# Optimization experiments

Hardware: AMD Instinct MI355X
Metric: run time of the kernel (lower is better)

## Reference

```python
import jax, jax.numpy as jnp
import numpy as np

B, N, K, G = 8, 16384, 16, 4
D_OUT = 128
CQ = CV = 64            # cv must equal d_out//2 for the lpe reshape to work
CQG, CVG = CQ // G, CV // G
C_LPE = D_OUT // (2 * G)  # = CVG = 16
BN_EPS = 1e-5


def setup_inputs() -> dict:
    key = jax.random.key(0)
    ks = jax.random.split(key, 8)
    xyz = jax.random.normal(ks[0], (B, N, 3), dtype=jnp.float32)
    query = jax.random.normal(ks[1], (B, CQ, N), dtype=jnp.float32)
    value = jax.random.normal(ks[2], (B, CV, N, 1), dtype=jnp.float32)
    neigh_idx = jax.random.randint(ks[3], (B, N, K), 0, N, dtype=jnp.int64)
    idx_base = (jnp.arange(B, dtype=jnp.int64) * N).reshape(B, 1, 1)
    lpe_W = jax.random.normal(ks[4], (C_LPE, 10), dtype=jnp.float32) * 0.1
    lpe_b = jnp.zeros((C_LPE,), dtype=jnp.float32)
    bn_gamma = jnp.ones((C_LPE,), dtype=jnp.float32)
    bn_beta = jnp.zeros((C_LPE,), dtype=jnp.float32)
    bn_mean = jnp.zeros((C_LPE,), dtype=jnp.float32)
    bn_var = jnp.ones((C_LPE,), dtype=jnp.float32)
    return {"xyz": xyz, "query": query, "value": value,
            "neigh_idx": neigh_idx, "idx_base": idx_base,
            "lpe_W": lpe_W, "lpe_b": lpe_b, "bn_gamma": bn_gamma,
            "bn_beta": bn_beta, "bn_mean": bn_mean, "bn_var": bn_var}


def _gtl_forward(xyz, query, value, neigh_idx, idx_base,
                 lpe_W, lpe_b, bn_gamma, bn_beta, bn_mean, bn_var):
    b, n, _ = xyz.shape
    k = neigh_idx.shape[-1]
    lq = query.reshape(b, G, CQG, n)                       # [b,g,cqg,n]
    lv = value.reshape(b, G, CVG, n)                       # [b,g,cvg,n]
    xyz_g = jnp.broadcast_to(xyz[:, None].transpose(0, 1, 3, 2), (b, G, 3, n))
    # temp channels: key(cqg) | value(cvg) | xyz(3)
    temp = jnp.concatenate([lq, lv, xyz_g], axis=2)        # [b,g,c,n]
    c = temp.shape[2]
    # flat gather honoring idx_base (batch offsets into b*n)
    flat_idx = (neigh_idx + idx_base).reshape(-1)          # [b*n*k]
    pc_flat = temp.transpose(1, 0, 3, 2).reshape(G, b * n, c)
    feat = pc_flat[:, flat_idx, :].reshape(G, b, n, k, c)
    feat = feat.transpose(1, 0, 4, 2, 3)                   # [b,g,c,n,k]
    lk = feat[:, :, :CQG]                                  # [b,g,cqg,n,k]
    lv_n = feat[:, :, CQG:CQG + CVG]                       # [b,g,cvg,n,k]
    f_xyz = feat[:, :, -3:]                                # [b,g,3,n,k]
    # relative positional encoding -> [b,g,n,k,10]
    neighbor_xyz = f_xyz.transpose(0, 1, 3, 4, 2)          # [b,g,n,k,3]
    xyz_tile = jnp.broadcast_to(xyz[:, None, :, None, :], (b, G, n, k, 3))
    relative_xyz = xyz_tile - neighbor_xyz
    relative_dis = jnp.sqrt(jnp.sum(relative_xyz ** 2, axis=-1, keepdims=True))
    relf = jnp.concatenate([relative_dis, relative_xyz, xyz_tile, neighbor_xyz], axis=-1)
    # permute(0,4,2,1,3) then merge (g,k) -> conv input [b,10,n,g*k]
    relf = relf.transpose(0, 4, 2, 1, 3).reshape(b, 10, n, G * k)
    y = jnp.einsum('oc,bcnm->bonm', lpe_W, relf) + lpe_b[None, :, None, None]
    inv_std = bn_gamma / jnp.sqrt(bn_var + BN_EPS)
    y = (y - bn_mean[None, :, None, None]) * inv_std[None, :, None, None] \
        + bn_beta[None, :, None, None]
    y = jax.nn.relu(y)
    f_enc = y.reshape(b, C_LPE, n, G, k).transpose(0, 3, 1, 2, 4)  # [b,g,cvg,n,k]
    # elementwise attention over neighbors
    la = jax.nn.softmax(jnp.sum(lq[..., None] * lk, axis=2), axis=-1)  # [b,g,n,k]
    lv_cat = jnp.concatenate([lv_n, f_enc], axis=2)        # [b,g,2*cvg,n,k]
    out = jnp.sum(la[:, :, None] * lv_cat, axis=-1).reshape(b, -1, n, 1)
    # attention centrality: scatter-add over neighbor indices
    idx_flat = jnp.broadcast_to(neigh_idx[:, None], (b, G, n, k)).reshape(b, G, n * k)
    att_flat = la.reshape(b, G, n * k)
    centrality = jnp.zeros((b, G, n), dtype=la.dtype).at[
        jnp.arange(b)[:, None, None], jnp.arange(G)[None, :, None], idx_flat
    ].add(att_flat)
    return out, f_enc, centrality


def reference(xyz, query, value, neigh_idx, idx_base,
              lpe_W, lpe_b, bn_gamma, bn_beta, bn_mean, bn_var):
    return _gtl_forward(xyz, query, value, neigh_idx, idx_base,
                        lpe_W, lpe_b, bn_gamma, bn_beta, bn_mean, bn_var)
```

## Files before the change

### kernel.cpp

```cpp
#include <hip/hip_runtime.h>

#define B_    8
#define N_    16384
#define K_    16
#define G_    4
#define CQ_   64
#define CV_   64
#define CQG_  16
#define CVG_  16
#define CLPE_ 16
#define NT_   (B_*G_*N_)

typedef float f4v __attribute__((ext_vector_type(4)));

static __device__ __forceinline__ void nt_store4(float* p, float a, float b,
                                                 float c, float d) {
    f4v v = {a, b, c, d};
    __builtin_nontemporal_store(v, (f4v*)p);
}
static __device__ __forceinline__ void nt_store1(float* p, float a) {
    __builtin_nontemporal_store(a, p);
}

__global__ __launch_bounds__(256) void gtl_prep(
    const float* __restrict__ query,
    const float* __restrict__ value,
    const float* __restrict__ xyz,
    float4* __restrict__ qT4,
    float4* __restrict__ vT4,
    float4* __restrict__ xyz4,
    float*  __restrict__ cent)
{
    __shared__ float sq[CQG_][68];
    __shared__ float sv[CVG_][68];

    const int t    = threadIdx.x;
    const int bg   = blockIdx.x >> 8;
    const int tile = blockIdx.x & 255;
    const int n0   = tile << 6;
    const int g    = bg & (G_ - 1);
    const int b    = bg >> 2;

    const int row = t >> 6;
    const int col = t & 63;

    const float* qb = query + (size_t)b*CQ_*N_ + (size_t)g*CQG_*N_ + n0;
    const float* vb = value + (size_t)b*CV_*N_ + (size_t)g*CVG_*N_ + n0;

    #pragma unroll
    for (int cc = 0; cc < 4; ++cc) {
        const int c = (cc << 2) + row;
        sq[c][col] = qb[(size_t)c*N_ + col];
        sv[c][col] = vb[(size_t)c*N_ + col];
    }

    if (t < 64) {
        cent[(size_t)bg*N_ + n0 + t] = 0.f;
        if (g == 0) {
            const size_t pp = (size_t)b*N_ + n0 + t;
            xyz4[pp] = make_float4(xyz[pp*3+0], xyz[pp*3+1], xyz[pp*3+2], 0.f);
        }
    }

    __syncthreads();

    const int p    = t >> 2;
    const int quad = t & 3;
    const int cb   = quad << 2;
    const float4 oq = make_float4(sq[cb+0][p], sq[cb+1][p], sq[cb+2][p], sq[cb+3][p]);
    const float4 ov = make_float4(sv[cb+0][p], sv[cb+1][p], sv[cb+2][p], sv[cb+3][p]);
    const size_t o = ((size_t)bg*N_ + n0 + p)*4 + quad;
    qT4[o] = oq;
    vT4[o] = ov;
}

__global__ __launch_bounds__(256) void gtl_main(
    const float*  __restrict__ qT,
    const float*  __restrict__ vT,
    const float4* __restrict__ xyz4,
    const int*    __restrict__ nidx,
    const float*  __restrict__ lpeW,
    const float*  __restrict__ lpeB,
    const float*  __restrict__ bnG,
    const float*  __restrict__ bnB,
    const float*  __restrict__ bnM,
    const float*  __restrict__ bnV,
    float* __restrict__ out,
    float* __restrict__ fenc,
    float* __restrict__ cent)
{
    __shared__ float4 sA[CLPE_];
    __shared__ float4 sB[CLPE_];

    const int t = threadIdx.x;
    if (t < CLPE_) {
        const float scale = bnG[t] * rsqrtf(bnV[t] + 1e-5f);
        const float shift = (lpeB[t] - bnM[t]) * scale + bnB[t];
        const float w0 = lpeW[t*10+0];
        const float w1 = lpeW[t*10+1], w2 = lpeW[t*10+2], w3 = lpeW[t*10+3];
        const float w4 = lpeW[t*10+4], w5 = lpeW[t*10+5], w6 = lpeW[t*10+6];
        const float w7 = lpeW[t*10+7], w8 = lpeW[t*10+8], w9 = lpeW[t*10+9];
        sA[t] = make_float4(scale*(w1+w4), scale*(w2+w5), scale*(w3+w6), shift);
        sB[t] = make_float4(scale*(w7-w1), scale*(w8-w2), scale*(w9-w3), scale*w0);
    }
    __syncthreads();

    const int wid  = blockIdx.x;
    const int xcd  = wid & 7;
    const int slot = wid >> 3;
    const int bg   = (xcd << 2) | (slot >> 6);
    const int n    = ((slot & 63) << 8) | t;
    const int b    = bg >> 2;

    int idx[K_];
    {
        const int4* ip = (const int4*)(nidx + (size_t)(b*N_ + n) * K_);
        #pragma unroll
        for (int q4 = 0; q4 < K_/4; ++q4) {
            const int4 v = ip[q4];
            idx[q4*4+0] = v.x; idx[q4*4+1] = v.y;
            idx[q4*4+2] = v.z; idx[q4*4+3] = v.w;
        }
    }

    const float4* qslab = (const float4*)(qT + (size_t)bg * N_ * 16);
    const float4 lq0 = qslab[(size_t)n*4+0];
    const float4 lq1 = qslab[(size_t)n*4+1];
    const float4 lq2 = qslab[(size_t)n*4+2];
    const float4 lq3 = qslab[(size_t)n*4+3];

    float la[K_];
    #pragma unroll 4
    for (int k = 0; k < K_; ++k) {
        const float4* qj = qslab + (size_t)idx[k]*4;
        const float4 a = qj[0], bq = qj[1], cq = qj[2], dq = qj[3];
        float s;
        s = lq0.x*a.x;            s = fmaf(lq0.y, a.y, s);
        s = fmaf(lq0.z, a.z, s);  s = fmaf(lq0.w, a.w, s);
        s = fmaf(lq1.x, bq.x, s); s = fmaf(lq1.y, bq.y, s);
        s = fmaf(lq1.z, bq.z, s); s = fmaf(lq1.w, bq.w, s);
        s = fmaf(lq2.x, cq.x, s); s = fmaf(lq2.y, cq.y, s);
        s = fmaf(lq2.z, cq.z, s); s = fmaf(lq2.w, cq.w, s);
        s = fmaf(lq3.x, dq.x, s); s = fmaf(lq3.y, dq.y, s);
        s = fmaf(lq3.z, dq.z, s); s = fmaf(lq3.w, dq.w, s);
        la[k] = s;
    }

    float m = la[0];
    #pragma unroll
    for (int k = 1; k < K_; ++k) m = fmaxf(m, la[k]);
    float ssum = 0.f;
    #pragma unroll
    for (int k = 0; k < K_; ++k) { const float e = __expf(la[k] - m); la[k] = e; ssum += e; }
    const float inv = 1.f / ssum;
    #pragma unroll
    for (int k = 0; k < K_; ++k) la[k] *= inv;

    {
        float* cb = cent + (size_t)bg * N_;
        #pragma unroll
        for (int k = 0; k < K_; ++k) atomicAdd(cb + idx[k], la[k]);
    }

    const float4 cpt = xyz4[(size_t)b*N_ + n];
    float basec[CLPE_];
    #pragma unroll
    for (int c = 0; c < CLPE_; ++c) {
        const float4 a = sA[c];
        basec[c] = fmaf(a.x, cpt.x, fmaf(a.y, cpt.y, fmaf(a.z, cpt.z, a.w)));
    }

    const float4* vslab = (const float4*)(vT + (size_t)bg * N_ * 16);
    float4 nbr[K_];
    float accV[CVG_];
    #pragma unroll
    for (int c = 0; c < CVG_; ++c) accV[c] = 0.f;

    #pragma unroll 2
    for (int k = 0; k < K_; ++k) {
        const int j = idx[k];
        const float4 p = xyz4[(size_t)b*N_ + j];
        const float rx = cpt.x - p.x, ry = cpt.y - p.y, rz = cpt.z - p.z;
        const float d  = sqrtf(fmaf(rx,rx, fmaf(ry,ry, rz*rz)));
        nbr[k] = make_float4(p.x, p.y, p.z, d);
        const float w = la[k];
        const float4* vj = vslab + (size_t)j*4;
        const float4 v0 = vj[0], v1 = vj[1], v2 = vj[2], v3 = vj[3];
        accV[0]  = fmaf(w, v0.x, accV[0]);  accV[1]  = fmaf(w, v0.y, accV[1]);
        accV[2]  = fmaf(w, v0.z, accV[2]);  accV[3]  = fmaf(w, v0.w, accV[3]);
        accV[4]  = fmaf(w, v1.x, accV[4]);  accV[5]  = fmaf(w, v1.y, accV[5]);
        accV[6]  = fmaf(w, v1.z, accV[6]);  accV[7]  = fmaf(w, v1.w, accV[7]);
        accV[8]  = fmaf(w, v2.x, accV[8]);  accV[9]  = fmaf(w, v2.y, accV[9]);
        accV[10] = fmaf(w, v2.z, accV[10]); accV[11] = fmaf(w, v2.w, accV[11]);
        accV[12] = fmaf(w, v3.x, accV[12]); accV[13] = fmaf(w, v3.y, accV[13]);
        accV[14] = fmaf(w, v3.z, accV[14]); accV[15] = fmaf(w, v3.w, accV[15]);
    }

    float* fe = fenc + ((size_t)bg * CLPE_ * N_ + n) * K_;
    float* ob = out  + (size_t)bg * (CVG_ + CLPE_) * N_ + n;

    #pragma unroll 2
    for (int c = 0; c < CLPE_; ++c) {
        const float4 wB = sB[c];
        const float base = basec[c];
        float e[K_];
        float acc = 0.f;
        #pragma unroll
        for (int k = 0; k < K_; ++k) {
            const float4 p = nbr[k];
            float tt = base;
            tt = fmaf(wB.x, p.x, tt);
            tt = fmaf(wB.y, p.y, tt);
            tt = fmaf(wB.z, p.z, tt);
            tt = fmaf(wB.w, p.w, tt);
            tt = fmaxf(tt, 0.f);
            e[k] = tt;
            acc  = fmaf(la[k], tt, acc);
        }
        float* fo = fe + (size_t)c * (N_ * K_);
        nt_store4(fo + 0,  e[0],  e[1],  e[2],  e[3]);
        nt_store4(fo + 4,  e[4],  e[5],  e[6],  e[7]);
        nt_store4(fo + 8,  e[8],  e[9],  e[10], e[11]);
        nt_store4(fo + 12, e[12], e[13], e[14], e[15]);
        nt_store1(ob + (size_t)(CVG_ + c) * N_, acc);
    }

    #pragma unroll
    for (int c = 0; c < CVG_; ++c) nt_store1(ob + (size_t)c * N_, accV[c]);
}

__global__ __launch_bounds__(256) void gtl_fallback(
    const float* __restrict__ xyz,
    const float* __restrict__ query,
    const float* __restrict__ value,
    const int*   __restrict__ nidx,
    const float* __restrict__ lpeW,
    const float* __restrict__ lpeB,
    const float* __restrict__ bnG,
    const float* __restrict__ bnB,
    const float* __restrict__ bnM,
    const float* __restrict__ bnV,
    float* __restrict__ out,
    float* __restrict__ fenc,
    float* __restrict__ cent)
{
    __shared__ float4 sA[CLPE_];
    __shared__ float4 sB[CLPE_];
    const int t = threadIdx.x;
    if (t < CLPE_) {
        const float scale = bnG[t] * rsqrtf(bnV[t] + 1e-5f);
        const float shift = (lpeB[t] - bnM[t]) * scale + bnB[t];
        const float w0 = lpeW[t*10+0];
        const float w1 = lpeW[t*10+1], w2 = lpeW[t*10+2], w3 = lpeW[t*10+3];
        const float w4 = lpeW[t*10+4], w5 = lpeW[t*10+5], w6 = lpeW[t*10+6];
        const float w7 = lpeW[t*10+7], w8 = lpeW[t*10+8], w9 = lpeW[t*10+9];
        sA[t] = make_float4(scale*(w1+w4), scale*(w2+w5), scale*(w3+w6), shift);
        sB[t] = make_float4(scale*(w7-w1), scale*(w8-w2), scale*(w9-w3), scale*w0);
    }
    __syncthreads();
    const int gid = blockIdx.x * 256 + t;
    const int n   = gid & (N_ - 1);
    const int bg  = gid >> 14;
    const int g   = bg & (G_ - 1);
    const int b   = bg >> 2;
    const float cx = xyz[(size_t)(b*N_ + n)*3 + 0];
    const float cy = xyz[(size_t)(b*N_ + n)*3 + 1];
    const float cz = xyz[(size_t)(b*N_ + n)*3 + 2];
    int idx[K_];
    const int4* ip = (const int4*)(nidx + (size_t)(b*N_ + n) * K_);
    #pragma unroll
    for (int q4 = 0; q4 < K_/4; ++q4) {
        const int4 v = ip[q4];
        idx[q4*4+0] = v.x; idx[q4*4+1] = v.y; idx[q4*4+2] = v.z; idx[q4*4+3] = v.w;
    }
    const float* qb = query + (size_t)b*CQ_*N_ + (size_t)g*CQG_*N_;
    float lq[CQG_];
    #pragma unroll
    for (int c = 0; c < CQG_; ++c) lq[c] = qb[(size_t)c*N_ + n];
    float la[K_];
    #pragma unroll 4
    for (int k = 0; k < K_; ++k) {
        const float* qj = qb + idx[k];
        float s = 0.f;
        #pragma unroll
        for (int c = 0; c < CQG_; ++c) s = fmaf(lq[c], qj[(size_t)c*N_], s);
        la[k] = s;
    }
    float m = la[0];
    #pragma unroll
    for (int k = 1; k < K_; ++k) m = fmaxf(m, la[k]);
    float ssum = 0.f;
    #pragma unroll
    for (int k = 0; k < K_; ++k) { const float e = __expf(la[k] - m); la[k] = e; ssum += e; }
    const float inv = 1.f / ssum;
    #pragma unroll
    for (int k = 0; k < K_; ++k) la[k] *= inv;
    float* cb = cent + (size_t)bg * N_;
    #pragma unroll
    for (int k = 0; k < K_; ++k) atomicAdd(cb + idx[k], la[k]);
    float basec[CLPE_];
    #pragma unroll
    for (int c = 0; c < CLPE_; ++c) {
        const float4 a = sA[c];
        basec[c] = fmaf(a.x, cx, fmaf(a.y, cy, fmaf(a.z, cz, a.w)));
    }
    const float* vb = value + (size_t)b*CV_*N_ + (size_t)g*CVG_*N_;
    float accV[CVG_], accE[CLPE_];
    #pragma unroll
    for (int c = 0; c < CLPE_; ++c) { accV[c] = 0.f; accE[c] = 0.f; }
    float* fe = fenc + ((size_t)bg * CLPE_ * N_ + n) * K_;
    #pragma unroll 2
    for (int k = 0; k < K_; ++k) {
        const int j = idx[k];
        const float nx = xyz[(size_t)(b*N_ + j)*3 + 0];
        const float ny = xyz[(size_t)(b*N_ + j)*3 + 1];
        const float nz = xyz[(size_t)(b*N_ + j)*3 + 2];
        const float rx = cx - nx, ry = cy - ny, rz = cz - nz;
        const float d  = sqrtf(rx*rx + ry*ry + rz*rz);
        const float w  = la[k];
        const float* vj = vb + j;
        #pragma unroll
        for (int c = 0; c < CLPE_; ++c) {
            const float4 bb = sB[c];
            float e = basec[c];
            e = fmaf(bb.x, nx, e); e = fmaf(bb.y, ny, e);
            e = fmaf(bb.z, nz, e); e = fmaf(bb.w, d,  e);
            e = fmaxf(e, 0.f);
            fe[(size_t)c*(N_*K_) + k] = e;
            accE[c] = fmaf(w, e, accE[c]);
            accV[c] = fmaf(w, vj[(size_t)c*N_], accV[c]);
        }
    }
    float* ob = out + (size_t)bg * (CVG_ + CLPE_) * N_ + n;
    #pragma unroll
    for (int c = 0; c < CVG_; ++c)  ob[(size_t)c*N_]        = accV[c];
    #pragma unroll
    for (int c = 0; c < CLPE_; ++c) ob[(size_t)(CVG_+c)*N_] = accE[c];
}

extern "C" void kernel_launch(void* const* d_in, const int* in_sizes, int n_in,
                              void* d_out, int out_size, void* d_ws, size_t ws_size,
                              hipStream_t stream) {
    (void)in_sizes; (void)n_in; (void)out_size;

    const float* xyz   = (const float*)d_in[0];
    const float* query = (const float*)d_in[1];
    const float* value = (const float*)d_in[2];
    const int*   nidx  = (const int*)  d_in[3];
    const float* lpeW  = (const float*)d_in[5];
    const float* lpeB  = (const float*)d_in[6];
    const float* bnG   = (const float*)d_in[7];
    const float* bnB   = (const float*)d_in[8];
    const float* bnM   = (const float*)d_in[9];
    const float* bnV   = (const float*)d_in[10];

    float* out  = (float*)d_out;
    float* fenc = out  + (size_t)B_ * (G_*(CVG_+CLPE_)) * N_;
    float* cent = fenc + (size_t)B_ * G_ * CLPE_ * N_ * K_;

    const size_t qT_bytes   = (size_t)NT_ * 16 * sizeof(float);
    const size_t vT_bytes   = qT_bytes;
    const size_t xyz4_bytes = (size_t)B_ * N_ * sizeof(float4);
    const size_t need = qT_bytes + vT_bytes + xyz4_bytes;

    if (ws_size >= need) {
        float*  qT   = (float*)d_ws;
        float*  vT   = qT + (size_t)NT_ * 16;
        float4* xyz4 = (float4*)(vT + (size_t)NT_ * 16);
        const int prep_grid = NT_ / 64;
        const int main_grid = NT_ / 256;
        hipLaunchKernelGGL(gtl_prep, dim3(prep_grid), dim3(256), 0, stream,
                           query, value, xyz, (float4*)qT, (float4*)vT, xyz4, cent);
        hipLaunchKernelGGL(gtl_main, dim3(main_grid), dim3(256), 0, stream,
                           qT, vT, xyz4, nidx, lpeW, lpeB, bnG, bnB, bnM, bnV,
                           out, fenc, cent);
    } else {
        hipMemsetAsync(cent, 0, sizeof(float) * (size_t)B_ * G_ * N_, stream);
        hipLaunchKernelGGL(gtl_fallback, dim3(NT_/256), dim3(256), 0, stream,
                           xyz, query, value, nidx, lpeW, lpeB, bnG, bnB, bnM, bnV,
                           out, fenc, cent);
    }
}
```

Baseline: 1.232 ms.

## Store gathered key/value features as fp16 in one interleaved 64-byte record

The prep kernel now converts query and value channels to half precision and packs both into a single 64-byte record per point, replacing two separate fp32 tables. It also drops the shared-memory transpose in favour of per-thread strided reads. The main kernel gathers one cache-line-sized record per neighbor and widens the value loop unroll, aiming to halve random gather traffic. This costs fp16 rounding on keys and values, which could exceed the accuracy tolerance.

```diff
diff --git a/kernel.cpp b/kernel.cpp
--- a/kernel.cpp
+++ b/kernel.cpp
@@ -1,4 +1,5 @@
 #include <hip/hip_runtime.h>
+#include <hip/hip_fp16.h>
 
 #define B_    8
 #define N_    16384
@@ -22,61 +23,57 @@
     __builtin_nontemporal_store(a, p);
 }
 
+union QV { uint4 u; __half2 h[4]; };
+
 __global__ __launch_bounds__(256) void gtl_prep(
     const float* __restrict__ query,
     const float* __restrict__ value,
     const float* __restrict__ xyz,
-    float4* __restrict__ qT4,
-    float4* __restrict__ vT4,
+    uint4*  __restrict__ qvT,
     float4* __restrict__ xyz4,
     float*  __restrict__ cent)
 {
-    __shared__ float sq[CQG_][68];
-    __shared__ float sv[CVG_][68];
-
-    const int t    = threadIdx.x;
-    const int bg   = blockIdx.x >> 8;
-    const int tile = blockIdx.x & 255;
-    const int n0   = tile << 6;
-    const int g    = bg & (G_ - 1);
-    const int b    = bg >> 2;
-
-    const int row = t >> 6;
-    const int col = t & 63;
-
-    const float* qb = query + (size_t)b*CQ_*N_ + (size_t)g*CQG_*N_ + n0;
-    const float* vb = value + (size_t)b*CV_*N_ + (size_t)g*CVG_*N_ + n0;
-
-    #pragma unroll
-    for (int cc = 0; cc < 4; ++cc) {
-        const int c = (cc << 2) + row;
-        sq[c][col] = qb[(size_t)c*N_ + col];
-        sv[c][col] = vb[(size_t)c*N_ + col];
-    }
-
-    if (t < 64) {
-        cent[(size_t)bg*N_ + n0 + t] = 0.f;
-        if (g == 0) {
-            const size_t pp = (size_t)b*N_ + n0 + t;
-            xyz4[pp] = make_float4(xyz[pp*3+0], xyz[pp*3+1], xyz[pp*3+2], 0.f);
-        }
-    }
-
-    __syncthreads();
-
-    const int p    = t >> 2;
-    const int quad = t & 3;
-    const int cb   = quad << 2;
-    const float4 oq = make_float4(sq[cb+0][p], sq[cb+1][p], sq[cb+2][p], sq[cb+3][p]);
-    const float4 ov = make_float4(sv[cb+0][p], sv[cb+1][p], sv[cb+2][p], sv[cb+3][p]);
-    const size_t o = ((size_t)bg*N_ + n0 + p)*4 + quad;
-    qT4[o] = oq;
-    vT4[o] = ov;
+    const int gid = blockIdx.x * 256 + threadIdx.x;
+    const int n   = gid & (N_ - 1);
+    const int bg  = gid >> 14;
+    const int g   = bg & (G_ - 1);
+    const int b   = bg >> 2;
+
+    const float* qb = query + (size_t)b*CQ_*N_ + (size_t)g*CQG_*N_ + n;
+    const float* vb = value + (size_t)b*CV_*N_ + (size_t)g*CVG_*N_ + n;
+
+    uint u[16];
+    #pragma unroll
+    for (int i = 0; i < 8; ++i) {
+        const float a0 = qb[(size_t)(2*i+0)*N_];
+        const float a1 = qb[(size_t)(2*i+1)*N_];
+        const __half2 h = __floats2half2_rn(a0, a1);
+        u[i] = *(const uint*)&h;
+    }
+    #pragma unroll
+    for (int i = 0; i < 8; ++i) {
+        const float a0 = vb[(size_t)(2*i+0)*N_];
+        const float a1 = vb[(size_t)(2*i+1)*N_];
+        const __half2 h = __floats2half2_rn(a0, a1);
+        u[8+i] = *(const uint*)&h;
+    }
+
+    uint4* o = qvT + (size_t)gid * 4;
+    o[0] = make_uint4(u[0],  u[1],  u[2],  u[3]);
+    o[1] = make_uint4(u[4],  u[5],  u[6],  u[7]);
+    o[2] = make_uint4(u[8],  u[9],  u[10], u[11]);
+    o[3] = make_uint4(u[12], u[13], u[14], u[15]);
+
+    cent[gid] = 0.f;
+
+    if (g == 0) {
+        const size_t pp = (size_t)b*N_ + n;
+        xyz4[pp] = make_float4(xyz[pp*3+0], xyz[pp*3+1], xyz[pp*3+2], 0.f);
+    }
 }
 
 __global__ __launch_bounds__(256) void gtl_main(
-    const float*  __restrict__ qT,
-    const float*  __restrict__ vT,
+    const uint4*  __restrict__ qvT,
     const float4* __restrict__ xyz4,
     const int*    __restrict__ nidx,
     const float*  __restrict__ lpeW,
@@ -123,26 +120,45 @@
         }
     }
 
-    const float4* qslab = (const float4*)(qT + (size_t)bg * N_ * 16);
-    const float4 lq0 = qslab[(size_t)n*4+0];
-    const float4 lq1 = qslab[(size_t)n*4+1];
-    const float4 lq2 = qslab[(size_t)n*4+2];
-    const float4 lq3 = qslab[(size_t)n*4+3];
+    const uint4* qvslab = qvT + (size_t)bg * N_ * 4;
+
+    float lq[CQG_];
+    {
+        QV cA, cB;
+        cA.u = qvslab[(size_t)n*4+0];
+        cB.u = qvslab[(size_t)n*4+1];
+        #pragma unroll
+        for (int i = 0; i < 4; ++i) {
+            const float2 f = __half22float2(cA.h[i]);
+            lq[2*i+0] = f.x; lq[2*i+1] = f.y;
+        }
+        #pragma unroll
+        for (int i = 0; i < 4; ++i) {
+            const float2 f = __half22float2(cB.h[i]);
+            lq[8+2*i+0] = f.x; lq[8+2*i+1] = f.y;
+        }
+    }
 
     float la[K_];
     #pragma unroll 4
     for (int k = 0; k < K_; ++k) {
-        const float4* qj = qslab + (size_t)idx[k]*4;
-        const float4 a = qj[0], bq = qj[1], cq = qj[2], dq = qj[3];
-        float s;
-        s = lq0.x*a.x;            s = fmaf(lq0.y, a.y, s);
-        s = fmaf(lq0.z, a.z, s);  s = fmaf(lq0.w, a.w, s);
-        s = fmaf(lq1.x, bq.x, s); s = fmaf(lq1.y, bq.y, s);
-        s = fmaf(lq1.z, bq.z, s); s = fmaf(lq1.w, bq.w, s);
-        s = fmaf(lq2.x, cq.x, s); s = fmaf(lq2.y, cq.y, s);
-        s = fmaf(lq2.z, cq.z, s); s = fmaf(lq2.w, cq.w, s);
-        s = fmaf(lq3.x, dq.x, s); s = fmaf(lq3.y, dq.y, s);
-        s = fmaf(lq3.z, dq.z, s); s = fmaf(lq3.w, dq.w, s);
+        const uint4* qj = qvslab + (size_t)idx[k]*4;
+        QV a, b2;
+        a.u  = qj[0];
+        b2.u = qj[1];
+        float s = 0.f;
+        #pragma unroll
+        for (int i = 0; i < 4; ++i) {
+            const float2 f = __half22float2(a.h[i]);
+            s = fmaf(lq[2*i+0], f.x, s);
+            s = fmaf(lq[2*i+1], f.y, s);
+        }
+        #pragma unroll
+        for (int i = 0; i < 4; ++i) {
+            const float2 f = __half22float2(b2.h[i]);
+            s = fmaf(lq[8+2*i+0], f.x, s);
+            s = fmaf(lq[8+2*i+1], f.y, s);
+        }
         la[k] = s;
     }
 
@@ -170,13 +186,12 @@
         basec[c] = fmaf(a.x, cpt.x, fmaf(a.y, cpt.y, fmaf(a.z, cpt.z, a.w)));
     }
 
-    const float4* vslab = (const float4*)(vT + (size_t)bg * N_ * 16);
     float4 nbr[K_];
     float accV[CVG_];
     #pragma unroll
     for (int c = 0; c < CVG_; ++c) accV[c] = 0.f;
 
-    #pragma unroll 2
+    #pragma unroll 4
     for (int k = 0; k < K_; ++k) {
         const int j = idx[k];
         const float4 p = xyz4[(size_t)b*N_ + j];
@@ -184,16 +199,22 @@
         const float d  = sqrtf(fmaf(rx,rx, fmaf(ry,ry, rz*rz)));
         nbr[k] = make_float4(p.x, p.y, p.z, d);
         const float w = la[k];
-        const float4* vj = vslab + (size_t)j*4;
-        const float4 v0 = vj[0], v1 = vj[1], v2 = vj[2], v3 = vj[3];
-        accV[0]  = fmaf(w, v0.x, accV[0]);  accV[1]  = fmaf(w, v0.y, accV[1]);
-        accV[2]  = fmaf(w, v0.z, accV[2]);  accV[3]  = fmaf(w, v0.w, accV[3]);
-        accV[4]  = fmaf(w, v1.x, accV[4]);  accV[5]  = fmaf(w, v1.y, accV[5]);
-        accV[6]  = fmaf(w, v1.z, accV[6]);  accV[7]  = fmaf(w, v1.w, accV[7]);
-        accV[8]  = fmaf(w, v2.x, accV[8]);  accV[9]  = fmaf(w, v2.y, accV[9]);
-        accV[10] = fmaf(w, v2.z, accV[10]); accV[11] = fmaf(w, v2.w, accV[11]);
-        accV[12] = fmaf(w, v3.x, accV[12]); accV[13] = fmaf(w, v3.y, accV[13]);
-        accV[14] = fmaf(w, v3.z, accV[14]); accV[15] = fmaf(w, v3.w, accV[15]);
+        const uint4* vj = qvslab + (size_t)j*4 + 2;
+        QV v0, v1;
+        v0.u = vj[0];
+        v1.u = vj[1];
+        #pragma unroll
+        for (int i = 0; i < 4; ++i) {
+            const float2 f = __half22float2(v0.h[i]);
+            accV[2*i+0] = fmaf(w, f.x, accV[2*i+0]);
+            accV[2*i+1] = fmaf(w, f.y, accV[2*i+1]);
+        }
+        #pragma unroll
+        for (int i = 0; i < 4; ++i) {
+            const float2 f = __half22float2(v1.h[i]);
+            accV[8+2*i+0] = fmaf(w, f.x, accV[8+2*i+0]);
+            accV[8+2*i+1] = fmaf(w, f.y, accV[8+2*i+1]);
+        }
     }
 
     float* fe = fenc + ((size_t)bg * CLPE_ * N_ + n) * K_;
@@ -358,25 +379,23 @@
     float* fenc = out  + (size_t)B_ * (G_*(CVG_+CLPE_)) * N_;
     float* cent = fenc + (size_t)B_ * G_ * CLPE_ * N_ * K_;
 
-    const size_t qT_bytes   = (size_t)NT_ * 16 * sizeof(float);
-    const size_t vT_bytes   = qT_bytes;
+    const size_t qv_bytes   = (size_t)NT_ * 64;
     const size_t xyz4_bytes = (size_t)B_ * N_ * sizeof(float4);
-    const size_t need = qT_bytes + vT_bytes + xyz4_bytes;
+    const size_t need = qv_bytes + xyz4_bytes;
+
+    const int grid = NT_ / 256;
 
     if (ws_size >= need) {
-        float*  qT   = (float*)d_ws;
-        float*  vT   = qT + (size_t)NT_ * 16;
-        float4* xyz4 = (float4*)(vT + (size_t)NT_ * 16);
-        const int prep_grid = NT_ / 64;
-        const int main_grid = NT_ / 256;
-        hipLaunchKernelGGL(gtl_prep, dim3(prep_grid), dim3(256), 0, stream,
-                           query, value, xyz, (float4*)qT, (float4*)vT, xyz4, cent);
-        hipLaunchKernelGGL(gtl_main, dim3(main_grid), dim3(256), 0, stream,
-                           qT, vT, xyz4, nidx, lpeW, lpeB, bnG, bnB, bnM, bnV,
+        uint4*  qvT  = (uint4*)d_ws;
+        float4* xyz4 = (float4*)((char*)d_ws + qv_bytes);
+        hipLaunchKernelGGL(gtl_prep, dim3(grid), dim3(256), 0, stream,
+                           query, value, xyz, qvT, xyz4, cent);
+        hipLaunchKernelGGL(gtl_main, dim3(grid), dim3(256), 0, stream,
+                           qvT, xyz4, nidx, lpeW, lpeB, bnG, bnB, bnM, bnV,
                            out, fenc, cent);
     } else {
         hipMemsetAsync(cent, 0, sizeof(float) * (size_t)B_ * G_ * N_, stream);
-        hipLaunchKernelGGL(gtl_fallback, dim3(NT_/256), dim3(256), 0, stream,
+        hipLaunchKernelGGL(gtl_fallback, dim3(grid), dim3(256), 0, stream,
                            xyz, query, value, nidx, lpeW, lpeB, bnG, bnB, bnM, bnV,
                            out, fenc, cent);
     }
```

Measured after the change: 1.204 ms. 2.3% less time.
